# Kernel tuning notes

Hardware: AMD Instinct MI355X
Metric: run time of the kernel (lower is better)

## Reference

```python
import jax, jax.numpy as jnp
import numpy as np
import math

NUM_HEADS = 4
HIDDEN = 256
HEAD_DIM = HIDDEN // NUM_HEADS
NEG = jnp.finfo(jnp.float32).min


def setup_inputs() -> dict:
    key = jax.random.key(0)
    ks = jax.random.split(key, 8)
    B, Q, K = 4, 2048, 2048
    q_hidden_states = jax.random.normal(ks[0], (B, Q, HIDDEN), dtype=jnp.float32)
    k_hidden_states = jax.random.normal(ks[1], (B, K, HIDDEN), dtype=jnp.float32)
    attention_mask = jnp.zeros((B, 1, Q, K), dtype=jnp.float32)
    align_mask = jax.random.randint(ks[2], (B, K, Q), 0, 2, dtype=jnp.int32)
    s = 1.0 / math.sqrt(HIDDEN)
    Wq = jax.random.normal(ks[3], (HIDDEN, HIDDEN), dtype=jnp.float32) * s
    Wk = jax.random.normal(ks[4], (HIDDEN, HIDDEN), dtype=jnp.float32) * s
    Wv = jax.random.normal(ks[5], (HIDDEN, HIDDEN), dtype=jnp.float32) * s
    Wo = jax.random.normal(ks[6], (HIDDEN, HIDDEN), dtype=jnp.float32) * s
    return {"q_hidden_states": q_hidden_states, "k_hidden_states": k_hidden_states,
            "attention_mask": attention_mask, "align_mask": align_mask,
            "Wq": Wq, "Wk": Wk, "Wv": Wv, "Wo": Wo}


def reference(q_hidden_states, k_hidden_states, attention_mask, align_mask, Wq, Wk, Wv, Wo):
    B, Q, _ = q_hidden_states.shape
    K = k_hidden_states.shape[1]
    # torch Linear: y = x @ W.T  -> [B, S, H, D]
    q = (q_hidden_states @ Wq.T).reshape(B, Q, NUM_HEADS, HEAD_DIM)
    k = (k_hidden_states @ Wk.T).reshape(B, K, NUM_HEADS, HEAD_DIM)
    v = (k_hidden_states @ Wv.T).reshape(B, K, NUM_HEADS, HEAD_DIM)
    # scores: [B, H, Q, K]
    scores = jnp.einsum('bqhd,bkhd->bhqk', q, k) / math.sqrt(HEAD_DIM)
    # additive mask + clamp to finfo min
    scores = jnp.maximum(scores + attention_mask, NEG)
    # align_mask: (B, K, Q) -> (B, 1, Q, K); masked_fill where == 0
    am = jnp.transpose(align_mask, (0, 2, 1))[:, None, :, :]
    scores = jnp.where(am == 0, NEG, scores)
    scores = jnp.maximum(scores, NEG)
    probs = jax.nn.softmax(scores.astype(jnp.float32), axis=-1).astype(q.dtype)
    attn = jnp.einsum('bhqk,bkhd->bqhd', probs, v).reshape(B, Q, HIDDEN)
    return attn @ Wo.T
```

## Files before the change

### kernel.cpp

```cpp
#include <hip/hip_runtime.h>

#define NEGF -3.402823466e38f
#define MASKED_F -3.38953139e38f
#define LOG2E 1.44269504088896f
#define DEFER_THR 8.0f

typedef __attribute__((ext_vector_type(8))) short bf16x8;
typedef __attribute__((ext_vector_type(4))) float f32x4;
typedef __attribute__((ext_vector_type(4))) unsigned short u16x4;
typedef __attribute__((ext_vector_type(2))) unsigned int u32x2;

__device__ __forceinline__ unsigned short f2bf(float f) {
  unsigned u = __builtin_bit_cast(unsigned, f);
  u += 0x7fffu + ((u >> 16) & 1u);
  return (unsigned short)(u >> 16);
}

#define GLOAD_LDS16(gsrc, ldst)                                                     \
  __builtin_amdgcn_global_load_lds(                                                 \
      (const __attribute__((address_space(1))) void*)(gsrc),                        \
      (__attribute__((address_space(3))) void*)(ldst), 16, 0, 0)

#define OFF_QH  0u
#define OFF_KH  2097152u
#define OFF_W   4194304u
#define OFF_QP  4456448u
#define OFF_KP  6553600u
#define OFF_VT  8650752u
#define OFF_ATT 10747904u
#define OFF_BM  12845056u
#define OFF_FLAG 13893632u
#define USHORT_USED 13893664u

__global__ __launch_bounds__(256) void k_convert(
    const float* __restrict__ qh, const float* __restrict__ kh,
    const float* __restrict__ w0, const float* __restrict__ w1,
    const float* __restrict__ w2, const float* __restrict__ w3,
    unsigned short* __restrict__ dst, int* __restrict__ flag) {
  int v = blockIdx.x * 256 + threadIdx.x;
  if (v == 0) *flag = 0;
  const float* src;
  if (v < 524288)       src = qh + (size_t)v * 4;
  else if (v < 1048576) src = kh + ((size_t)v - 524288) * 4;
  else {
    int t = v - 1048576;
    int which = t >> 14;
    const float* w = (which == 0) ? w0 : (which == 1) ? w1 : (which == 2) ? w2 : w3;
    src = w + (size_t)(t & 16383) * 4;
  }
  f32x4 x = *(const f32x4*)src;
  u16x4 o;
  o[0] = f2bf(x[0]); o[1] = f2bf(x[1]); o[2] = f2bf(x[2]); o[3] = f2bf(x[3]);
  *(u16x4*)(dst + (size_t)v * 4) = o;
}

__global__ __launch_bounds__(256) void k_maskaux(const int* __restrict__ al,
    const float* __restrict__ am, unsigned long long* __restrict__ bm,
    int* __restrict__ flag) {
  int bid = blockIdx.x;
  if (bid < 1024) {
    int wi = bid * 256 + threadIdx.x;
    int q = wi & 2047;
    int k64 = (wi >> 11) & 31;
    int b = wi >> 16;
    const int* base = al + ((size_t)(b * 2048 + k64 * 64)) * 2048 + q;
    unsigned long long word = 0;
#pragma unroll
    for (int k = 0; k < 64; ++k)
      if (base[(size_t)k * 2048] != 0) word |= 1ull << k;
    bm[wi] = word;
  } else {
    const f32x4* p = (const f32x4*)am;
    size_t tid = (size_t)(bid - 1024) * 256 + threadIdx.x;
    unsigned nz = 0;
#pragma unroll
    for (int j = 0; j < 16; ++j) {
      f32x4 v = p[tid + (size_t)j * 262144];
      nz |= (v[0] != 0.f) | (v[1] != 0.f) | (v[2] != 0.f) | (v[3] != 0.f);
    }
    if (__any(nz)) {
      if ((threadIdx.x & 63) == 0) atomicOr(flag, 1);
    }
  }
}

__global__ __launch_bounds__(256) void k_proj(unsigned short* __restrict__ ws) {
  int bid = blockIdx.x;
  int mat = bid / 512;
  int rem = bid - mat * 512;
  int mt = rem >> 2, nt = rem & 3;
  int tid = threadIdx.x, w = tid >> 6, lane = tid & 63;
  int l15 = lane & 15, l4 = lane >> 4;

  const unsigned short* X = ws + (mat == 0 ? OFF_QH : OFF_KH);
  const unsigned short* W = ws + OFF_W + (size_t)mat * 65536;

  int i0 = mt * 64 + w * 16;
  int arow = i0 + l15;
  int koff = l4 * 8;

  f32x4 acc[4] = {};
  for (int ks = 0; ks < 8; ++ks) {
    bf16x8 a = *(const bf16x8*)(X + (size_t)arow * 256 + ks * 32 + koff);
#pragma unroll
    for (int ct = 0; ct < 4; ++ct) {
      bf16x8 bb = *(const bf16x8*)(W + (size_t)(nt * 64 + ct * 16 + l15) * 256 + ks * 32 + koff);
      acc[ct] = __builtin_amdgcn_mfma_f32_16x16x32_bf16(a, bb, acc[ct], 0, 0, 0);
    }
  }

  unsigned short* Qp = ws + OFF_QP;
  unsigned short* Kp = ws + OFF_KP;
  unsigned short* Vt = ws + OFF_VT;
  int rbase = i0 + l4 * 4;
#pragma unroll
  for (int ct = 0; ct < 4; ++ct) {
#pragma unroll
    for (int r = 0; r < 4; ++r) {
      int row = rbase + r;
      int b = row >> 11, s = row & 2047;
      int d = ct * 16 + l15;
      float v = acc[ct][r];
      if (mat == 0)      Qp[((size_t)(b * 4 + nt) * 2048 + s) * 64 + d] = f2bf(v * (0.125f * LOG2E));
      else if (mat == 1) Kp[((size_t)(b * 4 + nt) * 2048 + s) * 64 + d] = f2bf(v);
      else               Vt[((size_t)(b * 4 + nt) * 64 + d) * 2048 + s] = f2bf(v);
    }
  }
}

template <int NS>
__global__ __launch_bounds__(256) void k_attn(unsigned short* __restrict__ ws,
    const float* __restrict__ am, const unsigned long long* __restrict__ bm,
    const int* __restrict__ amflag,
    float* __restrict__ po, float* __restrict__ pm, float* __restrict__ pl) {
  constexpr int LOG = (NS == 4) ? 2 : (NS == 2) ? 1 : 0;
  constexpr int SPAN = 2048 / NS;

  __shared__ __align__(16) unsigned short Kb[2][4096];
  __shared__ __align__(16) unsigned short Vb[2][4096];
  __shared__ __align__(16) unsigned short plds[4][1024];

  int bid = blockIdx.x;
  int sp = bid & (NS - 1);
  int qt = (bid >> LOG) & 31;
  int bh = bid >> (LOG + 5);
  int b = bh >> 2, h = bh & 3;
  int tid = threadIdx.x, w = tid >> 6, lane = tid & 63;
  int l15 = lane & 15, l4 = lane >> 4;
  int q0 = qt * 64 + w * 16;

  const bool hasam = (*amflag != 0);

  const unsigned short* Qp = ws + OFF_QP;
  const unsigned short* Kp = ws + OFF_KP + (size_t)bh * 2048 * 64;
  const unsigned short* Vt = ws + OFF_VT + (size_t)bh * 64 * 2048;
  const float* amq = am + ((size_t)(b * 2048 + q0 + l15)) * 2048;
  const unsigned long long* bmq = bm + (size_t)b * 65536 + q0 + l15;

  int srow = lane >> 3;
  int scol = ((lane & 7) ^ srow) * 8;
  int c0 = w * 2;

  bf16x8 qf0 = *(const bf16x8*)(Qp + ((size_t)bh * 2048 + q0 + l15) * 64 + l4 * 8);
  bf16x8 qf1 = *(const bf16x8*)(Qp + ((size_t)bh * 2048 + q0 + l15) * 64 + 32 + l4 * 8);

  f32x4 o[4] = {};
  float mrun = -__builtin_inff();
  float lpart = 0.f;
  int s0 = l4 * 4;

  int kk0 = sp * SPAN;
#pragma unroll
  for (int c2 = 0; c2 < 2; ++c2) {
    int c = c0 + c2;
    GLOAD_LDS16(Kp + (size_t)(kk0 + c * 8 + srow) * 64 + scol, &Kb[0][c * 512]);
    GLOAD_LDS16(Vt + (size_t)(c * 8 + srow) * 2048 + kk0 + scol, &Vb[0][c * 512]);
  }
  __syncthreads();

  int cur = 0;
  for (int kk = kk0; kk < kk0 + SPAN; kk += 64) {
    unsigned long long wbits = bmq[(size_t)(kk >> 6) * 2048];
    f32x4 a0{}, a1{}, a2{}, a3{};
    if (hasam) {
      a0 = *(const f32x4*)(amq + kk + 0 * 16 + s0);
      a1 = *(const f32x4*)(amq + kk + 1 * 16 + s0);
      a2 = *(const f32x4*)(amq + kk + 2 * 16 + s0);
      a3 = *(const f32x4*)(amq + kk + 3 * 16 + s0);
    }
    if (kk + 64 < kk0 + SPAN) {
#pragma unroll
      for (int c2 = 0; c2 < 2; ++c2) {
        int c = c0 + c2;
        GLOAD_LDS16(Kp + (size_t)(kk + 64 + c * 8 + srow) * 64 + scol, &Kb[cur ^ 1][c * 512]);
        GLOAD_LDS16(Vt + (size_t)(c * 8 + srow) * 2048 + (kk + 64) + scol, &Vb[cur ^ 1][c * 512]);
      }
    }

    f32x4 sfr[4];
    __builtin_amdgcn_s_setprio(1);
#pragma unroll
    for (int kt = 0; kt < 4; ++kt) {
      int row = kt * 16 + l15;
      int sw = l15 & 7;
      bf16x8 k0 = *(const bf16x8*)&Kb[cur][row * 64 + ((l4 ^ sw) * 8)];
      bf16x8 k1 = *(const bf16x8*)&Kb[cur][row * 64 + (((4 + l4) ^ sw) * 8)];
      f32x4 acc = {};
      acc = __builtin_amdgcn_mfma_f32_16x16x32_bf16(k0, qf0, acc, 0, 0, 0);
      acc = __builtin_amdgcn_mfma_f32_16x16x32_bf16(k1, qf1, acc, 0, 0, 0);
      sfr[kt] = acc;
    }
    __builtin_amdgcn_s_setprio(0);

    if (hasam) {
#pragma unroll
      for (int kt = 0; kt < 4; ++kt) {
        f32x4 a = (kt == 0) ? a0 : (kt == 1) ? a1 : (kt == 2) ? a2 : a3;
#pragma unroll
        for (int r = 0; r < 4; ++r) sfr[kt][r] = fmaf(a[r], LOG2E, sfr[kt][r]);
      }
    }

    float pmax = sfr[0][0];
#pragma unroll
    for (int kt = 0; kt < 4; ++kt)
#pragma unroll
      for (int r = 0; r < 4; ++r) pmax = fmaxf(pmax, sfr[kt][r]);
    pmax = fmaxf(pmax, __shfl_xor(pmax, 16));
    pmax = fmaxf(pmax, __shfl_xor(pmax, 32));

    if (__any(pmax > mrun + DEFER_THR)) {
      float mnew = fmaxf(mrun, pmax);
      float sfac = exp2f(mrun - mnew);
      mrun = mnew;
      lpart *= sfac;
#pragma unroll
      for (int r = 0; r < 4; ++r) {
        float sf = __shfl(sfac, l4 * 4 + r);
        o[0][r] *= sf; o[1][r] *= sf; o[2][r] *= sf; o[3][r] *= sf;
      }
    }

    unsigned blo = (unsigned)wbits, bhi = (unsigned)(wbits >> 32);
    float ls = 0.f;
#pragma unroll
    for (int kt = 0; kt < 4; ++kt) {
      unsigned tbits = ((kt & 2) ? bhi : blo) >> ((kt & 1) ? 16 + s0 : s0);
      float em[4];
#pragma unroll
      for (int r = 0; r < 4; ++r) {
        float e = exp2f(sfr[kt][r] - mrun);
        unsigned keep = 0u - ((tbits >> r) & 1u);
        em[r] = __builtin_bit_cast(float, __builtin_bit_cast(unsigned, e) & keep);
        ls += em[r];
      }
      unsigned lo, hi;
      asm("v_cvt_pk_bf16_f32 %0, %1, %2" : "=v"(lo) : "v"(em[0]), "v"(em[1]));
      asm("v_cvt_pk_bf16_f32 %0, %1, %2" : "=v"(hi) : "v"(em[2]), "v"(em[3]));
      int chunk = kt * 2 + (l4 >> 1);
      int addr = l15 * 64 + (((chunk) ^ (l15 & 7)) << 3) + ((l4 & 1) << 2);
      u32x2 pk; pk[0] = lo; pk[1] = hi;
      *(u32x2*)&plds[w][addr] = pk;
    }
    lpart += ls;

    __builtin_amdgcn_s_setprio(1);
#pragma unroll
    for (int ks = 0; ks < 2; ++ks) {
      int chnk = ks * 4 + l4;
      bf16x8 pa = *(const bf16x8*)&plds[w][l15 * 64 + ((chnk ^ (l15 & 7)) << 3)];
#pragma unroll
      for (int dt = 0; dt < 4; ++dt) {
        int row = dt * 16 + l15;
        bf16x8 vf = *(const bf16x8*)&Vb[cur][row * 64 + (((ks * 4 + l4) ^ (l15 & 7)) * 8)];
        o[dt] = __builtin_amdgcn_mfma_f32_16x16x32_bf16(pa, vf, o[dt], 0, 0, 0);
      }
    }
    __builtin_amdgcn_s_setprio(0);

    __syncthreads();
    cur ^= 1;
  }

  float lsum = lpart;
  lsum += __shfl_xor(lsum, 16);
  lsum += __shfl_xor(lsum, 32);

  if constexpr (NS == 1) {
    unsigned short* attnb = ws + OFF_ATT;
#pragma unroll
    for (int r = 0; r < 4; ++r) {
      float inv = 1.0f / __shfl(lsum, l4 * 4 + r);
      int qrow = q0 + l4 * 4 + r;
#pragma unroll
      for (int dt = 0; dt < 4; ++dt)
        attnb[(size_t)(b * 2048 + qrow) * 256 + h * 64 + dt * 16 + l15] = f2bf(o[dt][r] * inv);
    }
  } else {
    float* pob = po + (((size_t)sp * 16 + bh) * 2048) * 64;
#pragma unroll
    for (int r = 0; r < 4; ++r) {
      int qrow = q0 + l4 * 4 + r;
#pragma unroll
      for (int dt = 0; dt < 4; ++dt)
        pob[(size_t)qrow * 64 + dt * 16 + l15] = o[dt][r];
    }
    if (l4 == 0) {
      pm[(size_t)sp * 32768 + bh * 2048 + q0 + l15] = mrun;
      pl[(size_t)sp * 32768 + bh * 2048 + q0 + l15] = lsum;
    }
  }
}

template <int NS>
__global__ __launch_bounds__(256) void k_combine(const float* __restrict__ po,
    const float* __restrict__ pm, const float* __restrict__ pl,
    unsigned short* __restrict__ attnb) {
  int t = blockIdx.x * 256 + threadIdx.x;
  int d = t & 63;
  int row = t >> 6;

  float m[NS], l[NS];
  float M = -__builtin_inff();
#pragma unroll
  for (int sp = 0; sp < NS; ++sp) {
    m[sp] = pm[(size_t)sp * 32768 + row];
    l[sp] = pl[(size_t)sp * 32768 + row];
    M = fmaxf(M, m[sp]);
  }
  float denom = 0.f, acc = 0.f;
#pragma unroll
  for (int sp = 0; sp < NS; ++sp) {
    float wgt = exp2f(m[sp] - M);
    denom += l[sp] * wgt;
    acc += po[((size_t)sp * 32768 + row) * 64 + d] * wgt;
  }
  float val = acc / denom;
  int bh = row >> 11, qrow = row & 2047;
  int b = bh >> 2, h = bh & 3;
  attnb[((size_t)(b * 2048 + qrow)) * 256 + h * 64 + d] = f2bf(val);
}

__global__ __launch_bounds__(256) void k_oproj(const unsigned short* __restrict__ ws,
                                               float* __restrict__ out) {
  int bid = blockIdx.x;
  int mt = bid >> 2, nt = bid & 3;
  int tid = threadIdx.x, w = tid >> 6, lane = tid & 63;
  int l15 = lane & 15, l4 = lane >> 4;

  const unsigned short* A = ws + OFF_ATT;
  const unsigned short* W = ws + OFF_W + 3u * 65536u;
  int i0 = mt * 64 + w * 16;

  f32x4 acc[4] = {};
  for (int ks = 0; ks < 8; ++ks) {
    bf16x8 a = *(const bf16x8*)(A + (size_t)(i0 + l15) * 256 + ks * 32 + l4 * 8);
#pragma unroll
    for (int ct = 0; ct < 4; ++ct) {
      bf16x8 bb = *(const bf16x8*)(W + (size_t)(nt * 64 + ct * 16 + l15) * 256 + ks * 32 + l4 * 8);
      acc[ct] = __builtin_amdgcn_mfma_f32_16x16x32_bf16(a, bb, acc[ct], 0, 0, 0);
    }
  }
#pragma unroll
  for (int ct = 0; ct < 4; ++ct)
#pragma unroll
    for (int r = 0; r < 4; ++r)
      out[(size_t)(i0 + l4 * 4 + r) * 256 + nt * 64 + ct * 16 + l15] = acc[ct][r];
}

extern "C" void kernel_launch(void* const* d_in, const int* in_sizes, int n_in,
                              void* d_out, int out_size, void* d_ws, size_t ws_size,
                              hipStream_t stream) {
  const float* qh = (const float*)d_in[0];
  const float* kh = (const float*)d_in[1];
  const float* amask = (const float*)d_in[2];
  const int* alignm = (const int*)d_in[3];
  const float* Wq = (const float*)d_in[4];
  const float* Wk = (const float*)d_in[5];
  const float* Wv = (const float*)d_in[6];
  const float* Wo = (const float*)d_in[7];
  float* out = (float*)d_out;
  unsigned short* ws = (unsigned short*)d_ws;
  unsigned long long* bm = (unsigned long long*)(ws + OFF_BM);
  int* amflag = (int*)(ws + OFF_FLAG);

  k_convert<<<4352, 256, 0, stream>>>(qh, kh, Wq, Wk, Wv, Wo, ws, amflag);
  k_maskaux<<<2048, 256, 0, stream>>>(alignm, amask, bm, amflag);
  k_proj<<<1536, 256, 0, stream>>>(ws);

  size_t avail_f = (ws_size > (size_t)USHORT_USED * 2)
                       ? (ws_size - (size_t)USHORT_USED * 2) / 4 : 0;
  auto need = [](int ns) { return (size_t)ns * (2097152 + 65536); };
  int NSv = (avail_f >= need(2)) ? 2 : 1;
  float* po = (float*)(ws + USHORT_USED);
  float* pm = po + (size_t)NSv * 2097152;
  float* pl = pm + (size_t)NSv * 32768;

  if (NSv == 2) {
    k_attn<2><<<1024, 256, 0, stream>>>(ws, amask, bm, amflag, po, pm, pl);
    k_combine<2><<<8192, 256, 0, stream>>>(po, pm, pl, ws + OFF_ATT);
  } else {
    k_attn<1><<<512, 256, 0, stream>>>(ws, amask, bm, amflag, po, pm, pl);
  }
  k_oproj<<<512, 256, 0, stream>>>(ws, out);
}
```

Baseline: 129.5 us.

## Fuse activation fp32-to-bf16 conversion into projection and widen GEMM tiles

The conversion kernel now only converts the weights. The projection kernel reads fp32 activations directly and packs them to bf16 in registers, so the bf16 copy of the activations is no longer written to and read back from global memory. The projection and output-projection kernels each compute all four 64-column tiles per block, reusing the A fragment across 256 output columns with a 4x4 accumulator array. In exchange, block counts drop sharply (384 and 128 blocks) and register use grows, which may cut occupancy and parallelism.

```diff
diff --git a/kernel.cpp b/kernel.cpp
--- a/kernel.cpp
+++ b/kernel.cpp
@@ -21,8 +21,6 @@
       (const __attribute__((address_space(1))) void*)(gsrc),                        \
       (__attribute__((address_space(3))) void*)(ldst), 16, 0, 0)
 
-#define OFF_QH  0u
-#define OFF_KH  2097152u
 #define OFF_W   4194304u
 #define OFF_QP  4456448u
 #define OFF_KP  6553600u
@@ -32,26 +30,18 @@
 #define OFF_FLAG 13893632u
 #define USHORT_USED 13893664u
 
-__global__ __launch_bounds__(256) void k_convert(
-    const float* __restrict__ qh, const float* __restrict__ kh,
+__global__ __launch_bounds__(256) void k_wconvert(
     const float* __restrict__ w0, const float* __restrict__ w1,
     const float* __restrict__ w2, const float* __restrict__ w3,
-    unsigned short* __restrict__ dst, int* __restrict__ flag) {
+    unsigned short* __restrict__ ws, int* __restrict__ flag) {
   int v = blockIdx.x * 256 + threadIdx.x;
   if (v == 0) *flag = 0;
-  const float* src;
-  if (v < 524288)       src = qh + (size_t)v * 4;
-  else if (v < 1048576) src = kh + ((size_t)v - 524288) * 4;
-  else {
-    int t = v - 1048576;
-    int which = t >> 14;
-    const float* w = (which == 0) ? w0 : (which == 1) ? w1 : (which == 2) ? w2 : w3;
-    src = w + (size_t)(t & 16383) * 4;
-  }
-  f32x4 x = *(const f32x4*)src;
+  int which = v >> 14;
+  const float* w = (which == 0) ? w0 : (which == 1) ? w1 : (which == 2) ? w2 : w3;
+  f32x4 x = *(const f32x4*)(w + (size_t)(v & 16383) * 4);
   u16x4 o;
   o[0] = f2bf(x[0]); o[1] = f2bf(x[1]); o[2] = f2bf(x[2]); o[3] = f2bf(x[3]);
-  *(u16x4*)(dst + (size_t)v * 4) = o;
+  *(u16x4*)(ws + OFF_W + (size_t)v * 4) = o;
 }
 
 __global__ __launch_bounds__(256) void k_maskaux(const int* __restrict__ al,
@@ -84,29 +74,38 @@
   }
 }
 
-__global__ __launch_bounds__(256) void k_proj(unsigned short* __restrict__ ws) {
+__global__ __launch_bounds__(256) void k_proj(const float* __restrict__ qh,
+    const float* __restrict__ kh, unsigned short* __restrict__ ws) {
   int bid = blockIdx.x;
-  int mat = bid / 512;
-  int rem = bid - mat * 512;
-  int mt = rem >> 2, nt = rem & 3;
+  int mat = bid >> 7;
+  int mt = bid & 127;
   int tid = threadIdx.x, w = tid >> 6, lane = tid & 63;
   int l15 = lane & 15, l4 = lane >> 4;
 
-  const unsigned short* X = ws + (mat == 0 ? OFF_QH : OFF_KH);
+  const float* X = (mat == 0) ? qh : kh;
   const unsigned short* W = ws + OFF_W + (size_t)mat * 65536;
 
   int i0 = mt * 64 + w * 16;
   int arow = i0 + l15;
   int koff = l4 * 8;
 
-  f32x4 acc[4] = {};
+  f32x4 acc[4][4] = {};
   for (int ks = 0; ks < 8; ++ks) {
-    bf16x8 a = *(const bf16x8*)(X + (size_t)arow * 256 + ks * 32 + koff);
-#pragma unroll
-    for (int ct = 0; ct < 4; ++ct) {
-      bf16x8 bb = *(const bf16x8*)(W + (size_t)(nt * 64 + ct * 16 + l15) * 256 + ks * 32 + koff);
-      acc[ct] = __builtin_amdgcn_mfma_f32_16x16x32_bf16(a, bb, acc[ct], 0, 0, 0);
-    }
+    f32x4 x0 = *(const f32x4*)(X + (size_t)arow * 256 + ks * 32 + koff);
+    f32x4 x1 = *(const f32x4*)(X + (size_t)arow * 256 + ks * 32 + koff + 4);
+    union { unsigned u[4]; bf16x8 v; } au;
+    asm("v_cvt_pk_bf16_f32 %0, %1, %2" : "=v"(au.u[0]) : "v"(x0[0]), "v"(x0[1]));
+    asm("v_cvt_pk_bf16_f32 %0, %1, %2" : "=v"(au.u[1]) : "v"(x0[2]), "v"(x0[3]));
+    asm("v_cvt_pk_bf16_f32 %0, %1, %2" : "=v"(au.u[2]) : "v"(x1[0]), "v"(x1[1]));
+    asm("v_cvt_pk_bf16_f32 %0, %1, %2" : "=v"(au.u[3]) : "v"(x1[2]), "v"(x1[3]));
+    bf16x8 a = au.v;
+#pragma unroll
+    for (int nt = 0; nt < 4; ++nt)
+#pragma unroll
+      for (int ct = 0; ct < 4; ++ct) {
+        bf16x8 bb = *(const bf16x8*)(W + (size_t)(nt * 64 + ct * 16 + l15) * 256 + ks * 32 + koff);
+        acc[nt][ct] = __builtin_amdgcn_mfma_f32_16x16x32_bf16(a, bb, acc[nt][ct], 0, 0, 0);
+      }
   }
 
   unsigned short* Qp = ws + OFF_QP;
@@ -114,16 +113,19 @@
   unsigned short* Vt = ws + OFF_VT;
   int rbase = i0 + l4 * 4;
 #pragma unroll
-  for (int ct = 0; ct < 4; ++ct) {
-#pragma unroll
-    for (int r = 0; r < 4; ++r) {
-      int row = rbase + r;
-      int b = row >> 11, s = row & 2047;
-      int d = ct * 16 + l15;
-      float v = acc[ct][r];
-      if (mat == 0)      Qp[((size_t)(b * 4 + nt) * 2048 + s) * 64 + d] = f2bf(v * (0.125f * LOG2E));
-      else if (mat == 1) Kp[((size_t)(b * 4 + nt) * 2048 + s) * 64 + d] = f2bf(v);
-      else               Vt[((size_t)(b * 4 + nt) * 64 + d) * 2048 + s] = f2bf(v);
+  for (int nt = 0; nt < 4; ++nt) {
+#pragma unroll
+    for (int ct = 0; ct < 4; ++ct) {
+#pragma unroll
+      for (int r = 0; r < 4; ++r) {
+        int row = rbase + r;
+        int b = row >> 11, s = row & 2047;
+        int d = ct * 16 + l15;
+        float v = acc[nt][ct][r];
+        if (mat == 0)      Qp[((size_t)(b * 4 + nt) * 2048 + s) * 64 + d] = f2bf(v * (0.125f * LOG2E));
+        else if (mat == 1) Kp[((size_t)(b * 4 + nt) * 2048 + s) * 64 + d] = f2bf(v);
+        else               Vt[((size_t)(b * 4 + nt) * 64 + d) * 2048 + s] = f2bf(v);
+      }
     }
   }
 }
@@ -343,8 +345,7 @@
 
 __global__ __launch_bounds__(256) void k_oproj(const unsigned short* __restrict__ ws,
                                                float* __restrict__ out) {
-  int bid = blockIdx.x;
-  int mt = bid >> 2, nt = bid & 3;
+  int mt = blockIdx.x;
   int tid = threadIdx.x, w = tid >> 6, lane = tid & 63;
   int l15 = lane & 15, l4 = lane >> 4;
 
@@ -352,20 +353,24 @@
   const unsigned short* W = ws + OFF_W + 3u * 65536u;
   int i0 = mt * 64 + w * 16;
 
-  f32x4 acc[4] = {};
+  f32x4 acc[4][4] = {};
   for (int ks = 0; ks < 8; ++ks) {
     bf16x8 a = *(const bf16x8*)(A + (size_t)(i0 + l15) * 256 + ks * 32 + l4 * 8);
 #pragma unroll
-    for (int ct = 0; ct < 4; ++ct) {
-      bf16x8 bb = *(const bf16x8*)(W + (size_t)(nt * 64 + ct * 16 + l15) * 256 + ks * 32 + l4 * 8);
-      acc[ct] = __builtin_amdgcn_mfma_f32_16x16x32_bf16(a, bb, acc[ct], 0, 0, 0);
-    }
-  }
-#pragma unroll
-  for (int ct = 0; ct < 4; ++ct)
-#pragma unroll
-    for (int r = 0; r < 4; ++r)
-      out[(size_t)(i0 + l4 * 4 + r) * 256 + nt * 64 + ct * 16 + l15] = acc[ct][r];
+    for (int nt = 0; nt < 4; ++nt)
+#pragma unroll
+      for (int ct = 0; ct < 4; ++ct) {
+        bf16x8 bb = *(const bf16x8*)(W + (size_t)(nt * 64 + ct * 16 + l15) * 256 + ks * 32 + l4 * 8);
+        acc[nt][ct] = __builtin_amdgcn_mfma_f32_16x16x32_bf16(a, bb, acc[nt][ct], 0, 0, 0);
+      }
+  }
+#pragma unroll
+  for (int nt = 0; nt < 4; ++nt)
+#pragma unroll
+    for (int ct = 0; ct < 4; ++ct)
+#pragma unroll
+      for (int r = 0; r < 4; ++r)
+        out[(size_t)(i0 + l4 * 4 + r) * 256 + nt * 64 + ct * 16 + l15] = acc[nt][ct][r];
 }
 
 extern "C" void kernel_launch(void* const* d_in, const int* in_sizes, int n_in,
@@ -384,9 +389,9 @@
   unsigned long long* bm = (unsigned long long*)(ws + OFF_BM);
   int* amflag = (int*)(ws + OFF_FLAG);
 
-  k_convert<<<4352, 256, 0, stream>>>(qh, kh, Wq, Wk, Wv, Wo, ws, amflag);
+  k_wconvert<<<256, 256, 0, stream>>>(Wq, Wk, Wv, Wo, ws, amflag);
   k_maskaux<<<2048, 256, 0, stream>>>(alignm, amask, bm, amflag);
-  k_proj<<<1536, 256, 0, stream>>>(ws);
+  k_proj<<<384, 256, 0, stream>>>(qh, kh, ws);
 
   size_t avail_f = (ws_size > (size_t)USHORT_USED * 2)
                        ? (ws_size - (size_t)USHORT_USED * 2) / 4 : 0;
@@ -402,5 +407,5 @@
   } else {
     k_attn<1><<<512, 256, 0, stream>>>(ws, amask, bm, amflag, po, pm, pl);
   }
-  k_oproj<<<512, 256, 0, stream>>>(ws, out);
-}
+  k_oproj<<<128, 256, 0, stream>>>(ws, out);
+}
```

Measured after the change: 155.1 us. 1.2x slower.
